# Kernel optimization log

Measured on AMD Instinct MI355X. Metric: run time of the kernel, lower is better.

The kernel has to match this reference:

```python
import jax, jax.numpy as jnp
import numpy as np

N_HEADS = 16
HEAD_DIM = 64
ROPE_BASE = 10000.0


def _rope_cos_sin(T, d, dtype):
    # GPT-NeoX style: inv_freq over even indices, cos/sin duplicated to full head_dim
    inv_freq = 1.0 / (ROPE_BASE ** (jnp.arange(0, d, 2, dtype=jnp.float32) / d))
    freqs = jnp.arange(T, dtype=jnp.float32)[:, None] * inv_freq[None, :]  # [T, d/2]
    emb = jnp.concatenate([freqs, freqs], axis=-1)  # [T, d]
    return jnp.cos(emb).astype(dtype), jnp.sin(emb).astype(dtype)


def _rotate_half(x):
    x1, x2 = jnp.split(x, 2, axis=-1)
    return jnp.concatenate([-x2, x1], axis=-1)


def setup_inputs() -> dict:
    key = jax.random.key(0)
    k1, k2, k3 = jax.random.split(key, 3)
    B, T, C = 2, 2048, 1024
    x = jax.random.normal(k1, (B, T, C), dtype=jnp.float32)
    Wqkv = jax.random.normal(k2, (C, 3 * C), dtype=jnp.float32) * (1.0 / np.sqrt(C))
    Wout = jax.random.normal(k3, (C, C), dtype=jnp.float32) * (1.0 / np.sqrt(C))
    return {"x": x, "Wqkv": Wqkv, "Wout": Wout}


def reference(x, Wqkv, Wout):
    B, T, C = x.shape
    H, D = N_HEADS, HEAD_DIM
    qkv = (x @ Wqkv).reshape(B, T, 3, H, D)
    q, k, v = qkv[:, :, 0], qkv[:, :, 1], qkv[:, :, 2]  # [B,T,H,D]
    q = q.transpose(0, 2, 1, 3)  # [B,H,T,D]
    k = k.transpose(0, 2, 1, 3)
    v = v.transpose(0, 2, 1, 3)
    cos, sin = _rope_cos_sin(T, D, x.dtype)  # [T,D]
    cos = cos[None, None]
    sin = sin[None, None]
    q = q * cos + _rotate_half(q) * sin
    k = k * cos + _rotate_half(k) * sin
    scale = 1.0 / np.sqrt(D)
    scores = jnp.einsum("bhqd,bhkd->bhqk", q, k) * scale  # [B,H,T,T]
    causal = jnp.tril(jnp.ones((T, T), dtype=bool))
    scores = jnp.where(causal[None, None], scores, jnp.finfo(scores.dtype).min)
    attn = jax.nn.softmax(scores, axis=-1)
    out = jnp.einsum("bhqk,bhkd->bhqd", attn, v)  # [B,H,T,D]
    out = out.transpose(0, 2, 1, 3).reshape(B, T, C)
    return out @ Wout
```

## Files before the change

### kernel.cpp

```cpp
#include <hip/hip_runtime.h>


#define B_  2
#define T_  2048
#define C_  1024
#define H_  16
#define D_  64
#define N3_ 3072

typedef unsigned short ushortx8 __attribute__((ext_vector_type(8)));
typedef unsigned short ushortx4 __attribute__((ext_vector_type(4)));
typedef short bf16x8 __attribute__((ext_vector_type(8)));
typedef float f32x4 __attribute__((ext_vector_type(4)));
typedef float f32x16 __attribute__((ext_vector_type(16)));
typedef unsigned int uintx2 __attribute__((ext_vector_type(2)));

__device__ __forceinline__ unsigned short f2bf(float f) {
  union { float f; unsigned u; } v; v.f = f;
  unsigned r = v.u + 0x7FFFu + ((v.u >> 16) & 1u);
  return (unsigned short)(r >> 16);
}
__device__ __forceinline__ float bf2f(unsigned short h) {
  union { unsigned u; float f; } v; v.u = ((unsigned)h) << 16;
  return v.f;
}
__device__ __forceinline__ unsigned cvtpk_bf16(float lo, float hi) {
  unsigned r; asm("v_cvt_pk_bf16_f32 %0, %1, %2" : "=v"(r) : "v"(lo), "v"(hi));
  return r;
}
__device__ __forceinline__ void gload_lds16(const void* g, void* l) {
  __builtin_amdgcn_global_load_lds((const __attribute__((address_space(1))) void*)g,
                                   (__attribute__((address_space(3))) void*)l,
                                   16, 0, 0);
}

__global__ __launch_bounds__(256) void cvt_x_kernel(const float* __restrict__ x,
                                                    unsigned short* __restrict__ xb) {
  size_t i = ((size_t)blockIdx.x * 256 + threadIdx.x) * 4;
  const float4 v = *(const float4*)(x + i);
  ushortx4 o;
  o[0] = f2bf(v.x); o[1] = f2bf(v.y); o[2] = f2bf(v.z); o[3] = f2bf(v.w);
  *(ushortx4*)(xb + i) = o;
}

__global__ __launch_bounds__(256) void tconv_kernel(const float* __restrict__ W,
                                                    unsigned short* __restrict__ WT,
                                                    int K, int N) {
  __shared__ float tile[32][33];
  const int n0 = blockIdx.x * 32, k0 = blockIdx.y * 32;
  const int tx = threadIdx.x & 31, ty = threadIdx.x >> 5;
#pragma unroll
  for (int i = 0; i < 4; ++i)
    tile[ty + i * 8][tx] = W[(size_t)(k0 + ty + i * 8) * N + n0 + tx];
  __syncthreads();
#pragma unroll
  for (int i = 0; i < 4; ++i)
    WT[(size_t)(n0 + ty + i * 8) * K + k0 + tx] = f2bf(tile[tx][ty + i * 8]);
}

template <int OUTF32>
__global__ __launch_bounds__(256) void gemm_bt_kernel(const unsigned short* __restrict__ A,
                                                      const unsigned short* __restrict__ BT,
                                                      void* __restrict__ Cptr,
                                                      int M, int N, int K) {
  __shared__ unsigned short Alds[128 * 64];
  __shared__ unsigned short Blds[128 * 64];
  const int tid = threadIdx.x;
  const int w = tid >> 6, l = tid & 63;
  const int wr = w >> 1, wc = w & 1;
  const int lg = l >> 4, lr = l & 15;
  const int m0 = blockIdx.y * 128, n0 = blockIdx.x * 128;
  const int lr8 = l >> 3;
  const int lc8 = (l & 7) ^ lr8;

  f32x4 acc[4][4];
#pragma unroll
  for (int i = 0; i < 4; ++i)
#pragma unroll
    for (int j = 0; j < 4; ++j) acc[i][j] = f32x4{0.f, 0.f, 0.f, 0.f};

  for (int k0 = 0; k0 < K; k0 += 64) {
    __syncthreads();
#pragma unroll
    for (int i = 0; i < 4; ++i) {
      const int ch = w * 4 + i;
      gload_lds16(A + (size_t)(m0 + ch * 8 + lr8) * K + k0 + lc8 * 8, &Alds[ch * 512]);
      gload_lds16(BT + (size_t)(n0 + ch * 8 + lr8) * K + k0 + lc8 * 8, &Blds[ch * 512]);
    }
    __syncthreads();
#pragma unroll
    for (int kc = 0; kc < 2; ++kc) {
      bf16x8 af[4], bfr[4];
#pragma unroll
      for (int mi = 0; mi < 4; ++mi) {
        const int row = wr * 64 + mi * 16 + lr;
        const int c16 = (kc * 4 + lg) ^ (row & 7);
        af[mi] = *(const bf16x8*)(&Alds[row * 64 + c16 * 8]);
      }
#pragma unroll
      for (int nj = 0; nj < 4; ++nj) {
        const int row = wc * 64 + nj * 16 + lr;
        const int c16 = (kc * 4 + lg) ^ (row & 7);
        bfr[nj] = *(const bf16x8*)(&Blds[row * 64 + c16 * 8]);
      }
#pragma unroll
      for (int mi = 0; mi < 4; ++mi)
#pragma unroll
        for (int nj = 0; nj < 4; ++nj)
          acc[mi][nj] = __builtin_amdgcn_mfma_f32_16x16x32_bf16(af[mi], bfr[nj], acc[mi][nj], 0, 0, 0);
    }
  }
#pragma unroll
  for (int mi = 0; mi < 4; ++mi)
#pragma unroll
    for (int nj = 0; nj < 4; ++nj)
#pragma unroll
      for (int j = 0; j < 4; ++j) {
        const int row = m0 + wr * 64 + mi * 16 + lg * 4 + j;
        const int col = n0 + wc * 64 + nj * 16 + lr;
        if (OUTF32) ((float*)Cptr)[(size_t)row * N + col] = acc[mi][nj][j];
        else ((unsigned short*)Cptr)[(size_t)row * N + col] = f2bf(acc[mi][nj][j]);
      }
}

__global__ __launch_bounds__(256) void rope_pack_kernel(const unsigned short* __restrict__ QKV,
                                                        unsigned short* __restrict__ Qp,
                                                        unsigned short* __restrict__ Kp) {
  const int tt = blockIdx.x, bh = blockIdx.y;
  const int b = bh >> 4, h = bh & 15;
  const int tid = threadIdx.x;
  const int half = tid >> 7;
  const int r = (tid >> 1) & 63;
  const int d0 = (tid & 1) * 16;
  const int t = tt * 64 + r;
  const unsigned short* src = QKV + (size_t)(b * T_ + t) * N3_ + half * C_ + h * D_;
  ushortx8 lo0 = *(const ushortx8*)(src + d0);
  ushortx8 lo1 = *(const ushortx8*)(src + d0 + 8);
  ushortx8 hi0 = *(const ushortx8*)(src + d0 + 32);
  ushortx8 hi1 = *(const ushortx8*)(src + d0 + 40);
  ushortx8 olo0, olo1, ohi0, ohi1;
  const float scale = half ? 1.0f : 0.18033688011112042f;
  const float tf = (float)t;
#pragma unroll
  for (int jj = 0; jj < 16; ++jj) {
    const int d = d0 + jj;
    const float invf = exp2f((float)d * -0.41524101186092036f);
    const float ang = tf * invf;
    const float c = cosf(ang), s = sinf(ang);
    const float xl = bf2f(jj < 8 ? lo0[jj] : lo1[jj - 8]);
    const float xh = bf2f(jj < 8 ? hi0[jj] : hi1[jj - 8]);
    const unsigned short rl = f2bf((xl * c - xh * s) * scale);
    const unsigned short rh = f2bf((xh * c + xl * s) * scale);
    if (jj < 8) { olo0[jj] = rl; ohi0[jj] = rh; }
    else        { olo1[jj - 8] = rl; ohi1[jj - 8] = rh; }
  }
  unsigned short* dst = (half ? Kp : Qp) + ((size_t)bh * T_ + t) * D_;
  *(ushortx8*)(dst + d0) = olo0;
  *(ushortx8*)(dst + d0 + 8) = olo1;
  *(ushortx8*)(dst + d0 + 32) = ohi0;
  *(ushortx8*)(dst + d0 + 40) = ohi1;
}

__global__ __launch_bounds__(256) void vtrans_kernel(const unsigned short* __restrict__ QKV,
                                                     unsigned short* __restrict__ Vt) {
  __shared__ unsigned short tile[64][72];
  const int tt = blockIdx.x, bh = blockIdx.y;
  const int b = bh >> 4, h = bh & 15;
  const int tid = threadIdx.x;
  {
    const int r = tid >> 2, seg = tid & 3;
    const unsigned short* src = QKV + (size_t)(b * T_ + tt * 64 + r) * N3_ + 2 * C_ + h * D_ + seg * 16;
    *(ushortx8*)(&tile[r][seg * 16]) = *(const ushortx8*)(src);
    *(ushortx8*)(&tile[r][seg * 16 + 8]) = *(const ushortx8*)(src + 8);
  }
  __syncthreads();
  {
    const int d = tid >> 2, ts = tid & 3;
    ushortx8 o0, o1;
#pragma unroll
    for (int i = 0; i < 8; ++i) { o0[i] = tile[ts * 16 + i][d]; o1[i] = tile[ts * 16 + 8 + i][d]; }
    unsigned short* dst = Vt + ((size_t)bh * D_ + d) * T_ + tt * 64 + ts * 16;
    *(ushortx8*)(dst) = o0;
    *(ushortx8*)(dst + 8) = o1;
  }
}

__global__ __launch_bounds__(256, 2) void attn7_kernel(const unsigned short* __restrict__ Qp,
                                                       const unsigned short* __restrict__ Kp,
                                                       const unsigned short* __restrict__ Vt,
                                                       unsigned short* __restrict__ Ob) {
  __shared__ unsigned short Klds[3][64 * 64];
  __shared__ unsigned short Vlds[3][64 * 64];
  const int tid = threadIdx.x, w = tid >> 6, l = tid & 63;
  const int lq = l & 31, hi = l >> 5;
  const int swz = lq & 7;
  const int bid = blockIdx.x;
  const int bh = bid & 31;
  const int pp = bid >> 5;
  const int p = (pp < 8) ? pp : 23 - pp;
  const int s = (w < 2) ? (2 * p + w) : (62 - 2 * p + (w - 2));
  const int q0 = s * 32;
  const int ntiles = 32 - p;
  const size_t koff = (size_t)bh * T_ * D_;
  const unsigned short* Kb = Kp + koff;
  const unsigned short* Vb = Vt + (size_t)bh * D_ * T_;

  const int lr8 = l >> 3;
  const int lc8 = (l & 7) ^ lr8;

  bf16x8 qf[4];
  {
    const unsigned short* qp = Qp + koff + (size_t)(q0 + lq) * D_ + hi * 8;
#pragma unroll
    for (int ds = 0; ds < 4; ++ds) qf[ds] = *(const bf16x8*)(qp + ds * 16);
  }
  f32x16 o0, o1;
#pragma unroll
  for (int r = 0; r < 16; ++r) { o0[r] = 0.f; o1[r] = 0.f; }
  float m = -3.0e38f, lden = 0.f;

#pragma unroll
  for (int i = 0; i < 2; ++i) {
    const int c = w * 2 + i;
    gload_lds16(Kb + (size_t)(c * 8 + lr8) * D_ + lc8 * 8, &Klds[0][c * 512]);
    gload_lds16(Vb + (size_t)(c * 8 + lr8) * T_ + lc8 * 8, &Vlds[0][c * 512]);
  }

  for (int kt = 0; kt < ntiles; ++kt) {
    const int cur = kt % 3;
    const int nxt = (kt + 1) % 3;
    const int ktn = (kt + 1 < ntiles) ? kt + 1 : kt;
    const int kvn = ktn * 64;
#pragma unroll
    for (int i = 0; i < 2; ++i) {
      const int c = w * 2 + i;
      gload_lds16(Kb + (size_t)(kvn + c * 8 + lr8) * D_ + lc8 * 8, &Klds[nxt][c * 512]);
      gload_lds16(Vb + (size_t)(c * 8 + lr8) * T_ + kvn + lc8 * 8, &Vlds[nxt][c * 512]);
    }
    asm volatile("s_waitcnt vmcnt(4)" ::: "memory");
    __builtin_amdgcn_s_barrier();
    __builtin_amdgcn_sched_barrier(0);

    const int kv0 = kt * 64;
    if (kv0 <= q0 + 31) {
      const unsigned short* KL = &Klds[cur][0];
      const unsigned short* VL = &Vlds[cur][0];
      f32x16 acc0, acc1;
#pragma unroll
      for (int r = 0; r < 16; ++r) { acc0[r] = 0.f; acc1[r] = 0.f; }
      __builtin_amdgcn_s_setprio(1);
#pragma unroll
      for (int ds = 0; ds < 4; ++ds) {
        const int slot = ((ds * 2 + hi) ^ swz) * 8;
        const bf16x8 kf0 = *(const bf16x8*)(&KL[(lq) * 64 + slot]);
        const bf16x8 kf1 = *(const bf16x8*)(&KL[(32 + lq) * 64 + slot]);
        acc0 = __builtin_amdgcn_mfma_f32_32x32x16_bf16(kf0, qf[ds], acc0, 0, 0, 0);
        acc1 = __builtin_amdgcn_mfma_f32_32x32x16_bf16(kf1, qf[ds], acc1, 0, 0, 0);
      }
      __builtin_amdgcn_s_setprio(0);
      if (kv0 + 63 > q0) {
        const int thr0 = q0 + lq - kv0;
        const int thr1 = thr0 - 32;
#pragma unroll
        for (int r = 0; r < 16; ++r) {
          const int kvloc = (r & 3) + 8 * (r >> 2) + 4 * hi;
          if (kvloc > thr0) acc0[r] = -3.0e38f;
          if (kvloc > thr1) acc1[r] = -3.0e38f;
        }
      }
      float mx[8];
#pragma unroll
      for (int i = 0; i < 8; ++i)
        mx[i] = fmaxf(fmaxf(acc0[i], acc0[i + 8]), fmaxf(acc1[i], acc1[i + 8]));
#pragma unroll
      for (int i = 0; i < 4; ++i) mx[i] = fmaxf(mx[i], mx[i + 4]);
      const float mloc = fmaxf(fmaxf(mx[0], mx[1]), fmaxf(mx[2], mx[3]));
      const uintx2 mp = __builtin_amdgcn_permlane32_swap(__float_as_uint(mloc), __float_as_uint(mloc), false, false);
      const float pm = fmaxf(__uint_as_float(mp.x), __uint_as_float(mp.y));
      const bool grow = pm > m + 8.0f;
      if (__any(grow)) {
        const float mn = grow ? pm : m;
        const float alpha = __builtin_amdgcn_exp2f(m - mn);
        m = mn;
        lden *= alpha;
#pragma unroll
        for (int r = 0; r < 16; ++r) { o0[r] *= alpha; o1[r] *= alpha; }
      }
      float p0[16], p1[16];
#pragma unroll
      for (int r = 0; r < 16; ++r) {
        p0[r] = __builtin_amdgcn_exp2f(acc0[r] - m);
        p1[r] = __builtin_amdgcn_exp2f(acc1[r] - m);
      }
      unsigned W0 = cvtpk_bf16(p0[0], p0[1]), W1 = cvtpk_bf16(p0[2], p0[3]);
      unsigned W2 = cvtpk_bf16(p0[4], p0[5]), W3 = cvtpk_bf16(p0[6], p0[7]);
      uintx2 Aa = __builtin_amdgcn_permlane32_swap(W0, W2, false, false);
      uintx2 Ab = __builtin_amdgcn_permlane32_swap(W1, W3, false, false);
      union { unsigned u[4]; bf16x8 v; } pfa0 = {{Aa.x, Ab.x, Aa.y, Ab.y}};
      W0 = cvtpk_bf16(p0[8], p0[9]);   W1 = cvtpk_bf16(p0[10], p0[11]);
      W2 = cvtpk_bf16(p0[12], p0[13]); W3 = cvtpk_bf16(p0[14], p0[15]);
      Aa = __builtin_amdgcn_permlane32_swap(W0, W2, false, false);
      Ab = __builtin_amdgcn_permlane32_swap(W1, W3, false, false);
      union { unsigned u[4]; bf16x8 v; } pfa1 = {{Aa.x, Ab.x, Aa.y, Ab.y}};
      W0 = cvtpk_bf16(p1[0], p1[1]);   W1 = cvtpk_bf16(p1[2], p1[3]);
      W2 = cvtpk_bf16(p1[4], p1[5]);   W3 = cvtpk_bf16(p1[6], p1[7]);
      Aa = __builtin_amdgcn_permlane32_swap(W0, W2, false, false);
      Ab = __builtin_amdgcn_permlane32_swap(W1, W3, false, false);
      union { unsigned u[4]; bf16x8 v; } pfb0 = {{Aa.x, Ab.x, Aa.y, Ab.y}};
      W0 = cvtpk_bf16(p1[8], p1[9]);   W1 = cvtpk_bf16(p1[10], p1[11]);
      W2 = cvtpk_bf16(p1[12], p1[13]); W3 = cvtpk_bf16(p1[14], p1[15]);
      Aa = __builtin_amdgcn_permlane32_swap(W0, W2, false, false);
      Ab = __builtin_amdgcn_permlane32_swap(W1, W3, false, false);
      union { unsigned u[4]; bf16x8 v; } pfb1 = {{Aa.x, Ab.x, Aa.y, Ab.y}};

      __builtin_amdgcn_s_setprio(1);
#pragma unroll
      for (int dt = 0; dt < 2; ++dt) {
        const int rowb = (dt * 32 + lq) * 64;
        const bf16x8 vf0 = *(const bf16x8*)(&VL[rowb + ((0 * 2 + hi) ^ swz) * 8]);
        const bf16x8 vf1 = *(const bf16x8*)(&VL[rowb + ((1 * 2 + hi) ^ swz) * 8]);
        const bf16x8 vf2 = *(const bf16x8*)(&VL[rowb + ((2 * 2 + hi) ^ swz) * 8]);
        const bf16x8 vf3 = *(const bf16x8*)(&VL[rowb + ((3 * 2 + hi) ^ swz) * 8]);
        if (dt == 0) {
          o0 = __builtin_amdgcn_mfma_f32_32x32x16_bf16(vf0, pfa0.v, o0, 0, 0, 0);
          o0 = __builtin_amdgcn_mfma_f32_32x32x16_bf16(vf1, pfa1.v, o0, 0, 0, 0);
          o0 = __builtin_amdgcn_mfma_f32_32x32x16_bf16(vf2, pfb0.v, o0, 0, 0, 0);
          o0 = __builtin_amdgcn_mfma_f32_32x32x16_bf16(vf3, pfb1.v, o0, 0, 0, 0);
        } else {
          o1 = __builtin_amdgcn_mfma_f32_32x32x16_bf16(vf0, pfa0.v, o1, 0, 0, 0);
          o1 = __builtin_amdgcn_mfma_f32_32x32x16_bf16(vf1, pfa1.v, o1, 0, 0, 0);
          o1 = __builtin_amdgcn_mfma_f32_32x32x16_bf16(vf2, pfb0.v, o1, 0, 0, 0);
          o1 = __builtin_amdgcn_mfma_f32_32x32x16_bf16(vf3, pfb1.v, o1, 0, 0, 0);
        }
      }
      __builtin_amdgcn_s_setprio(0);
      float sm[8];
#pragma unroll
      for (int i = 0; i < 8; ++i) sm[i] = (p0[i] + p0[i + 8]) + (p1[i] + p1[i + 8]);
#pragma unroll
      for (int i = 0; i < 4; ++i) sm[i] = sm[i] + sm[i + 4];
      const float sloc = (sm[0] + sm[1]) + (sm[2] + sm[3]);
      const uintx2 sp = __builtin_amdgcn_permlane32_swap(__float_as_uint(sloc), __float_as_uint(sloc), false, false);
      lden += __uint_as_float(sp.x) + __uint_as_float(sp.y);
    }
  }
  asm volatile("s_waitcnt vmcnt(0)" ::: "memory");

  const float rl = __builtin_amdgcn_rcpf(lden);
  const int b = bh >> 4, hh = bh & 15;
  unsigned short* orow = Ob + (size_t)(b * T_ + q0 + lq) * C_ + hh * D_ + 4 * hi;
#pragma unroll
  for (int rq = 0; rq < 4; ++rq) {
    ushortx4 ov0, ov1;
#pragma unroll
    for (int i = 0; i < 4; ++i) {
      ov0[i] = f2bf(o0[rq * 4 + i] * rl);
      ov1[i] = f2bf(o1[rq * 4 + i] * rl);
    }
    *(ushortx4*)(orow + rq * 8) = ov0;
    *(ushortx4*)(orow + 32 + rq * 8) = ov1;
  }
}

extern "C" void kernel_launch(void* const* d_in, const int* in_sizes, int n_in,
                              void* d_out, int out_size, void* d_ws, size_t ws_size,
                              hipStream_t stream) {
  const float* x = (const float*)d_in[0];
  const float* Wqkv = (const float*)d_in[1];
  const float* Wout = (const float*)d_in[2];
  float* out = (float*)d_out;
  char* ws = (char*)d_ws;
  unsigned short* Xb    = (unsigned short*)(ws);
  unsigned short* WqkvT = (unsigned short*)(ws + (8ull << 20));
  unsigned short* WoutT = (unsigned short*)(ws + (14ull << 20));
  unsigned short* QKVb  = (unsigned short*)(ws + (16ull << 20));
  unsigned short* Qp    = (unsigned short*)(ws + (40ull << 20));
  unsigned short* Kp    = (unsigned short*)(ws + (48ull << 20));
  unsigned short* Vt    = (unsigned short*)(ws + (56ull << 20));
  unsigned short* Ob    = (unsigned short*)(ws + (64ull << 20));

  cvt_x_kernel<<<4096, 256, 0, stream>>>(x, Xb);
  tconv_kernel<<<dim3(N3_ / 32, C_ / 32), 256, 0, stream>>>(Wqkv, WqkvT, C_, N3_);
  tconv_kernel<<<dim3(C_ / 32, C_ / 32), 256, 0, stream>>>(Wout, WoutT, C_, C_);
  gemm_bt_kernel<0><<<dim3(N3_ / 128, (B_ * T_) / 128), 256, 0, stream>>>(
      Xb, WqkvT, QKVb, B_ * T_, N3_, C_);
  rope_pack_kernel<<<dim3(T_ / 64, B_ * H_), 256, 0, stream>>>(QKVb, Qp, Kp);
  vtrans_kernel<<<dim3(T_ / 64, B_ * H_), 256, 0, stream>>>(QKVb, Vt);
  attn7_kernel<<<512, 256, 0, stream>>>(Qp, Kp, Vt, Ob);
  gemm_bt_kernel<1><<<dim3(C_ / 128, (B_ * T_) / 128), 256, 0, stream>>>(
      Ob, WoutT, out, B_ * T_, C_, C_);
}
```

Measured before the change: 127.4 us.

## Use 256x256 double-buffered 8-wave GEMM for QKV projection

Replaces the 128x128 tile GEMM for the QKV projection with a new 256x256-tile kernel running 512 threads. It double-buffers LDS, spreads the next tile's global-to-LDS loads across the compute phases, raises wave priority around the MFMA blocks, and swizzles block order so neighbouring blocks share data in cache. The aim is more data reuse per loaded byte and better hiding of load latency. The cost is 128 KB of LDS per block, which limits occupancy, and a launch of only 192 blocks, which may leave compute units idle.

```diff
diff --git a/kernel.cpp b/kernel.cpp
--- a/kernel.cpp
+++ b/kernel.cpp
@@ -56,6 +56,95 @@
 #pragma unroll
   for (int i = 0; i < 4; ++i)
     WT[(size_t)(n0 + ty + i * 8) * K + k0 + tx] = f2bf(tile[tx][ty + i * 8]);
+}
+
+__global__ __launch_bounds__(512, 2) void gemm256_kernel(const unsigned short* __restrict__ A,
+                                                         const unsigned short* __restrict__ BT,
+                                                         unsigned short* __restrict__ Cb,
+                                                         int M, int N, int K) {
+  __shared__ unsigned short Alds[2][256 * 64];
+  __shared__ unsigned short Blds[2][256 * 64];
+  const int tid = threadIdx.x, w = tid >> 6, l = tid & 63;
+  const int wm = w >> 2, wn = w & 3;
+  const int lg = l >> 4, lr = l & 15;
+  const int lr8 = l >> 3, lc8 = (l & 7) ^ lr8;
+  const int bid = blockIdx.x;
+  const int swz = (bid & 7) * 24 + (bid >> 3);
+  const int nbn = N >> 8;
+  const int bm = swz / nbn, bn = swz % nbn;
+  const int m0 = bm * 256, n0 = bn * 256;
+  const int NT = K >> 6;
+
+  f32x4 acc[8][4];
+#pragma unroll
+  for (int i = 0; i < 8; ++i)
+#pragma unroll
+    for (int j = 0; j < 4; ++j) acc[i][j] = f32x4{0.f, 0.f, 0.f, 0.f};
+
+  auto stage2 = [&](int b, int k0n, int ph) {
+    const int ca = w * 4 + ph;
+    gload_lds16(A + (size_t)(m0 + ca * 8 + lr8) * K + k0n + lc8 * 8, &Alds[b][ca * 512]);
+    gload_lds16(BT + (size_t)(n0 + ca * 8 + lr8) * K + k0n + lc8 * 8, &Blds[b][ca * 512]);
+  };
+#pragma unroll
+  for (int ph = 0; ph < 4; ++ph) stage2(0, 0, ph);
+
+  for (int kt = 0; kt < NT; ++kt) {
+    const int buf = kt & 1;
+    const unsigned short* AL = &Alds[buf][0];
+    const unsigned short* BL = &Blds[buf][0];
+    const int k0n = (kt + 1) * 64;
+    const bool more = (kt + 1 < NT);
+    if (more) {
+      stage2(buf ^ 1, k0n, 0);
+      asm volatile("s_waitcnt vmcnt(2)" ::: "memory");
+    } else {
+      asm volatile("s_waitcnt vmcnt(0)" ::: "memory");
+    }
+    __builtin_amdgcn_s_barrier();
+    __builtin_amdgcn_sched_barrier(0);
+    bf16x8 bfr[4][2];
+#pragma unroll
+    for (int nj = 0; nj < 4; ++nj)
+#pragma unroll
+      for (int kc = 0; kc < 2; ++kc) {
+        const int row = wn * 64 + nj * 16 + lr;
+        bfr[nj][kc] = *(const bf16x8*)(&BL[row * 64 + (((kc * 4 + lg) ^ (row & 7))) * 8]);
+      }
+#pragma unroll
+    for (int q = 0; q < 4; ++q) {
+      if (q > 0 && more) stage2(buf ^ 1, k0n, q);
+      bf16x8 afp[2][2];
+#pragma unroll
+      for (int mi2 = 0; mi2 < 2; ++mi2)
+#pragma unroll
+        for (int kc = 0; kc < 2; ++kc) {
+          const int row = wm * 128 + (q * 2 + mi2) * 16 + lr;
+          afp[mi2][kc] = *(const bf16x8*)(&AL[row * 64 + (((kc * 4 + lg) ^ (row & 7))) * 8]);
+        }
+      __builtin_amdgcn_s_setprio(1);
+#pragma unroll
+      for (int mi2 = 0; mi2 < 2; ++mi2)
+#pragma unroll
+        for (int nj = 0; nj < 4; ++nj)
+#pragma unroll
+          for (int kc = 0; kc < 2; ++kc)
+            acc[q * 2 + mi2][nj] = __builtin_amdgcn_mfma_f32_16x16x32_bf16(
+                afp[mi2][kc], bfr[nj][kc], acc[q * 2 + mi2][nj], 0, 0, 0);
+      __builtin_amdgcn_s_setprio(0);
+    }
+    __builtin_amdgcn_s_barrier();
+  }
+#pragma unroll
+  for (int mi = 0; mi < 8; ++mi)
+#pragma unroll
+    for (int nj = 0; nj < 4; ++nj)
+#pragma unroll
+      for (int j = 0; j < 4; ++j) {
+        const int row = m0 + wm * 128 + mi * 16 + lg * 4 + j;
+        const int col = n0 + wn * 64 + nj * 16 + lr;
+        Cb[(size_t)row * N + col] = f2bf(acc[mi][nj][j]);
+      }
 }
 
 template <int OUTF32>
@@ -382,7 +471,7 @@
   cvt_x_kernel<<<4096, 256, 0, stream>>>(x, Xb);
   tconv_kernel<<<dim3(N3_ / 32, C_ / 32), 256, 0, stream>>>(Wqkv, WqkvT, C_, N3_);
   tconv_kernel<<<dim3(C_ / 32, C_ / 32), 256, 0, stream>>>(Wout, WoutT, C_, C_);
-  gemm_bt_kernel<0><<<dim3(N3_ / 128, (B_ * T_) / 128), 256, 0, stream>>>(
+  gemm256_kernel<<<(B_ * T_ / 256) * (N3_ / 256), 512, 0, stream>>>(
       Xb, WqkvT, QKVb, B_ * T_, N3_, C_);
   rope_pack_kernel<<<dim3(T_ / 64, B_ * H_), 256, 0, stream>>>(QKVb, Qp, Kp);
   vtrans_kernel<<<dim3(T_ / 64, B_ * H_), 256, 0, stream>>>(QKVb, Vt);
```

Measured after the change: 139.3 us. 9.3% more time.
